# Kernel tuning notes

Hardware: AMD Instinct MI355X
Metric: run time of the kernel (lower is better)

Reference implementation:

```python
import jax, jax.numpy as jnp
import numpy as np

N_EMBED = 288
HEAD_SIZE = 32


def setup_inputs() -> dict:
    key = jax.random.key(0)
    kx, kk, kq, kv = jax.random.split(key, 4)
    B, T, C = 16, 2048, N_EMBED
    scale = 1.0 / np.sqrt(C)
    return {
        "x": jax.random.normal(kx, (B, T, C), dtype=jnp.float32),
        # Linear(n_embed, head_size, bias=False) weights, stored as [C, head_size]
        "Wk": jax.random.normal(kk, (C, HEAD_SIZE), dtype=jnp.float32) * scale,
        "Wq": jax.random.normal(kq, (C, HEAD_SIZE), dtype=jnp.float32) * scale,
        "Wv": jax.random.normal(kv, (C, HEAD_SIZE), dtype=jnp.float32) * scale,
    }


def reference(x, Wk, Wq, Wv):
    # x: [B, T, C]
    k = x @ Wk  # [B, T, hs]
    q = x @ Wq
    v = x @ Wv
    # NOTE: source computes k @ q^T (not q @ k^T) -- reproduce faithfully.
    weights = jnp.einsum("bth,bsh->bts", k, q) * (HEAD_SIZE ** -0.5)  # [B, T, T]
    T = x.shape[1]
    causal = jnp.tril(jnp.ones((T, T), dtype=bool))
    weights = jnp.where(causal, weights, -jnp.inf)
    weights = jax.nn.softmax(weights, axis=-1)
    return weights @ v  # [B, T, hs]
```

## Files before the change

kernel.cpp:

```cpp
#include <hip/hip_runtime.h>

typedef __bf16 bf16;
typedef __attribute__((ext_vector_type(8))) __bf16 bf16x8;
typedef __attribute__((ext_vector_type(4))) float f32x4;

#define BATCH 16
#define SEQ   2048
#define CEMB  288
#define HS    32
#define NROWS (BATCH * SEQ)

#define XSTR 296

__global__ __launch_bounds__(384, 3) void proj_kernel(
    const float* __restrict__ x, const float* __restrict__ Wk,
    const float* __restrict__ Wq, const float* __restrict__ Wv,
    bf16* __restrict__ Kx, bf16* __restrict__ Qm, bf16* __restrict__ VT)
{
    __shared__ __align__(16) bf16 Xl[32 * XSTR];

    const int tid  = threadIdx.x;
    const int wv   = tid >> 6;
    const int lane = tid & 63;
    const int quad = lane >> 4;
    const int ln   = lane & 15;
    const int dsel = wv >> 1;
    const int half = wv & 1;

    const float SCALE = 0.25519486439582695f;

    const float* Wsrc = (dsel == 0) ? Wk : ((dsel == 1) ? Wq : Wv);
    const float mul = (dsel == 0) ? SCALE : 1.0f;
    bf16x8 wfrag[9];
    for (int kc = 0; kc < 9; ++kc) {
        bf16x8 f;
#pragma unroll
        for (int j = 0; j < 8; ++j) {
            float w = Wsrc[(kc * 32 + quad * 8 + j) * HS + half * 16 + ln];
            f[j] = (bf16)(w * mul);
        }
        wfrag[kc] = f;
    }

    const int wgRowBase = blockIdx.x * 64;
    for (int it = 0; it < 2; ++it) {
        __syncthreads();
        const int rb = wgRowBase + it * 32;
#pragma unroll
        for (int i = 0; i < 6; ++i) {
            int f = tid + 384 * i;
            int row = f / 72;
            int c4  = f - row * 72;
            f32x4 v = ((const f32x4*)x)[(rb + row) * 72 + c4];
            bf16* d = &Xl[row * XSTR + c4 * 4];
            d[0] = (bf16)v[0]; d[1] = (bf16)v[1];
            d[2] = (bf16)v[2]; d[3] = (bf16)v[3];
        }
        __syncthreads();

#pragma unroll
        for (int m = 0; m < 2; ++m) {
            f32x4 acc = {0.f, 0.f, 0.f, 0.f};
#pragma unroll
            for (int kc = 0; kc < 9; ++kc) {
                bf16x8 a = *(const bf16x8*)&Xl[(m * 16 + ln) * XSTR + kc * 32 + quad * 8];
                acc = __builtin_amdgcn_mfma_f32_16x16x32_bf16(a, wfrag[kc], acc, 0, 0, 0);
            }
#pragma unroll
            for (int reg = 0; reg < 4; ++reg) {
                int gr = rb + m * 16 + quad * 4 + reg;
                bf16 val = (bf16)acc[reg];
                if (dsel == 0) {
                    Kx[gr * HS + half * 16 + ln] = val;
                } else if (dsel == 1) {
                    Qm[gr * HS + half * 16 + ln] = val;
                } else {
                    VT[(gr >> 11) * (HS * SEQ) + (half * 16 + ln) * SEQ + (gr & 2047)] = val;
                }
            }
        }
    }
}


__constant__ unsigned char MAP_TILE[40] = {
    4,5,6,7, 8,8,9,9, 10,10,11,11, 12,12,12, 13,13,13, 14,14,14, 15,15,15,
    3,7,11,15, 2,6,10,14, 1,5,9,13, 0,4,8,12 };
__constant__ unsigned char MAP_CHUNK[40] = {
    0,0,0,0, 0,1,0,1, 0,1,0,1, 0,1,2, 0,1,2, 0,1,2, 0,1,2,
    0,1,2,3, 0,1,2,3, 0,1,2,3, 0,1,2,3 };

__global__ __launch_bounds__(256, 4) void attn_kernel(
    const bf16* __restrict__ Kx, const bf16* __restrict__ Qm,
    const bf16* __restrict__ VT,
    float* __restrict__ Opart, float* __restrict__ Lpart)
{
    const int tid  = threadIdx.x;
    const int w    = tid >> 6;
    const int lane = tid & 63;
    const int quad = lane >> 4;
    const int ln   = lane & 15;

    const int bid   = blockIdx.x;
    const int u     = bid >> 4;
    const int b     = ((bid & 7) << 1) | ((bid >> 3) & 1);
    const int tile  = MAP_TILE[u];
    const int chunk = MAP_CHUNK[u];
    const int t0    = tile * 128;
    const int cs    = chunk * 512;
    const int ce    = min(cs + 512, t0 + 128);

    const bf16* Kb = Kx + b * SEQ * HS;
    const bf16* Qb = Qm + b * SEQ * HS;
    const bf16* Vb = VT + b * HS * SEQ;

    int tsub[2];
    bf16x8 kfrag[2];
#pragma unroll
    for (int m = 0; m < 2; ++m) {
        tsub[m] = t0 + w * 32 + m * 16;
        kfrag[m] = *(const bf16x8*)&Kb[(tsub[m] + ln) * HS + quad * 8];
    }
    bf16x8 ones;
#pragma unroll
    for (int j = 0; j < 8; ++j) ones[j] = (bf16)1.0f;

    const int qrow = 8 * (ln >> 2) + (ln & 3);
    const int t_row = ln;

    f32x4 Of[2][2] = {};
    f32x4 Lf[2]    = {};

    for (int s0 = cs; s0 < ce; s0 += 64) {
        if (s0 >= tsub[1] + 16) break;

        bf16x8 qfA[2], qfB[2];
#pragma unroll
        for (int c = 0; c < 2; ++c) {
            qfA[c] = *(const bf16x8*)&Qb[(s0 + 32 * c + qrow) * HS + quad * 8];
            qfB[c] = *(const bf16x8*)&Qb[(s0 + 32 * c + qrow + 4) * HS + quad * 8];
        }
        bf16x8 vf[2][2];
#pragma unroll
        for (int hb = 0; hb < 2; ++hb)
#pragma unroll
            for (int c = 0; c < 2; ++c)
                vf[hb][c] = *(const bf16x8*)&Vb[(hb * 16 + ln) * SEQ + s0 + c * 32 + quad * 8];

#pragma unroll
        for (int m = 0; m < 2; ++m) {
            const int t = tsub[m] + t_row;
#pragma unroll
            for (int c = 0; c < 2; ++c) {
                const int sb = s0 + 32 * c;
                if (sb >= tsub[m] + 16) continue;
                const bool diag = (sb + 31 > tsub[m]);

                f32x4 z = {0.f, 0.f, 0.f, 0.f};
                f32x4 SA = __builtin_amdgcn_mfma_f32_16x16x32_bf16(qfA[c], kfrag[m], z, 0, 0, 0);
                f32x4 SB = __builtin_amdgcn_mfma_f32_16x16x32_bf16(qfB[c], kfrag[m], z, 0, 0, 0);

                const int sAb = sb + 8 * quad;
                float pA[4], pB[4];
#pragma unroll
                for (int r = 0; r < 4; ++r) {
                    pA[r] = __builtin_amdgcn_exp2f(SA[r]);
                    pB[r] = __builtin_amdgcn_exp2f(SB[r]);
                    if (diag) {
                        pA[r] = (sAb + r     <= t) ? pA[r] : 0.0f;
                        pB[r] = (sAb + r + 4 <= t) ? pB[r] : 0.0f;
                    }
                }

                bf16x8 ap;
#pragma unroll
                for (int r = 0; r < 4; ++r) {
                    ap[r]     = (bf16)pA[r];
                    ap[r + 4] = (bf16)pB[r];
                }

                Of[m][0] = __builtin_amdgcn_mfma_f32_16x16x32_bf16(ap, vf[0][c], Of[m][0], 0, 0, 0);
                Of[m][1] = __builtin_amdgcn_mfma_f32_16x16x32_bf16(ap, vf[1][c], Of[m][1], 0, 0, 0);
                Lf[m]    = __builtin_amdgcn_mfma_f32_16x16x32_bf16(ap, ones,    Lf[m],    0, 0, 0);
            }
        }
    }

#pragma unroll
    for (int m = 0; m < 2; ++m) {
        if (cs >= tsub[m] + 16) continue;
#pragma unroll
        for (int reg = 0; reg < 4; ++reg) {
            int gr = b * SEQ + tsub[m] + quad * 4 + reg;
            float* od = Opart + ((size_t)chunk * NROWS + gr) * HS;
            od[ln]      = Of[m][0][reg];
            od[16 + ln] = Of[m][1][reg];
            if (ln == 0) Lpart[chunk * NROWS + gr] = Lf[m][reg];
        }
    }
}

__global__ __launch_bounds__(256) void combine_kernel(
    const float* __restrict__ Opart, const float* __restrict__ Lpart,
    float* __restrict__ out)
{
    int idx = blockIdx.x * 256 + threadIdx.x;
    int gr = idx >> 3, h4 = idx & 7;
    int t  = gr & 2047;
    int nc = (t >> 9) + 1;
    f32x4 acc = {0.f, 0.f, 0.f, 0.f};
    float l = 0.f;
    for (int c = 0; c < nc; ++c) {
        acc += ((const f32x4*)Opart)[((size_t)c * NROWS + gr) * 8 + h4];
        l   += Lpart[c * NROWS + gr];
    }
    f32x4 r = acc / l;
    ((f32x4*)out)[idx] = r;
}

extern "C" void kernel_launch(void* const* d_in, const int* in_sizes, int n_in,
                              void* d_out, int out_size, void* d_ws, size_t ws_size,
                              hipStream_t stream) {
    (void)in_sizes; (void)n_in; (void)out_size; (void)ws_size;
    const float* x  = (const float*)d_in[0];
    const float* Wk = (const float*)d_in[1];
    const float* Wq = (const float*)d_in[2];
    const float* Wv = (const float*)d_in[3];

    char* ws = (char*)d_ws;
    bf16*  Kx    = (bf16*)(ws);
    bf16*  Qm    = (bf16*)(ws + 2097152);
    bf16*  VT    = (bf16*)(ws + 4194304);
    float* Opart = (float*)(ws + 6291456);
    float* Lpart = (float*)(ws + 6291456 + 16777216);
    float* out   = (float*)d_out;

    hipLaunchKernelGGL(proj_kernel, dim3(512), dim3(384), 0, stream,
                       x, Wk, Wq, Wv, Kx, Qm, VT);
    hipLaunchKernelGGL(attn_kernel, dim3(640), dim3(256), 0, stream,
                       Kx, Qm, VT, Opart, Lpart);
    hipLaunchKernelGGL(combine_kernel, dim3(1024), dim3(256), 0, stream,
                       Opart, Lpart, out);
}
```

Measured before the change: 105.1 us.

## Use 1024-key split chunks and write unsplit rows directly to output

The key-axis split grows from 512 to 1024 columns, which cuts the number of (tile, chunk) work units from 40 to 24 per batch and the attention grid from 640 to 384 blocks. Tiles that fit in the first chunk now normalise and write straight to the output. The combine kernel only merges two partials for the second half of the sequence. This removes partial-buffer traffic and combine work, at the cost of fewer, longer blocks and possible load imbalance across CUs.

```diff
diff --git a/kernel.cpp b/kernel.cpp
--- a/kernel.cpp
+++ b/kernel.cpp
@@ -83,17 +83,18 @@
 }
 
 
-__constant__ unsigned char MAP_TILE[40] = {
-    4,5,6,7, 8,8,9,9, 10,10,11,11, 12,12,12, 13,13,13, 14,14,14, 15,15,15,
-    3,7,11,15, 2,6,10,14, 1,5,9,13, 0,4,8,12 };
-__constant__ unsigned char MAP_CHUNK[40] = {
-    0,0,0,0, 0,1,0,1, 0,1,0,1, 0,1,2, 0,1,2, 0,1,2, 0,1,2,
-    0,1,2,3, 0,1,2,3, 0,1,2,3, 0,1,2,3 };
+__constant__ unsigned char MAP_TILE[24] = {
+    7,8,9,10,11,12,13,14,15,15,
+    14,6, 13,5, 12,4, 11,3, 10,2, 9,1, 8,0 };
+__constant__ unsigned char MAP_CHUNK[24] = {
+    0,0,0,0,0,0,0,0,0,1,
+    1,0, 1,0, 1,0, 1,0, 1,0, 1,0, 1,0 };
 
 __global__ __launch_bounds__(256, 4) void attn_kernel(
     const bf16* __restrict__ Kx, const bf16* __restrict__ Qm,
     const bf16* __restrict__ VT,
-    float* __restrict__ Opart, float* __restrict__ Lpart)
+    float* __restrict__ Opart, float* __restrict__ Lpart,
+    float* __restrict__ out)
 {
     const int tid  = threadIdx.x;
     const int w    = tid >> 6;
@@ -107,8 +108,9 @@
     const int tile  = MAP_TILE[u];
     const int chunk = MAP_CHUNK[u];
     const int t0    = tile * 128;
-    const int cs    = chunk * 512;
-    const int ce    = min(cs + 512, t0 + 128);
+    const int cs    = chunk * 1024;
+    const int ce    = min(cs + 1024, t0 + 128);
+    const bool direct = (chunk == 0) && (t0 + 128 <= 1024);
 
     const bf16* Kb = Kx + b * SEQ * HS;
     const bf16* Qb = Qm + b * SEQ * HS;
@@ -189,13 +191,24 @@
 #pragma unroll
     for (int m = 0; m < 2; ++m) {
         if (cs >= tsub[m] + 16) continue;
-#pragma unroll
-        for (int reg = 0; reg < 4; ++reg) {
-            int gr = b * SEQ + tsub[m] + quad * 4 + reg;
-            float* od = Opart + ((size_t)chunk * NROWS + gr) * HS;
-            od[ln]      = Of[m][0][reg];
-            od[16 + ln] = Of[m][1][reg];
-            if (ln == 0) Lpart[chunk * NROWS + gr] = Lf[m][reg];
+        if (direct) {
+#pragma unroll
+            for (int reg = 0; reg < 4; ++reg) {
+                int gr = b * SEQ + tsub[m] + quad * 4 + reg;
+                float rl = 1.0f / Lf[m][reg];
+                float* od = out + (size_t)gr * HS;
+                od[ln]      = Of[m][0][reg] * rl;
+                od[16 + ln] = Of[m][1][reg] * rl;
+            }
+        } else {
+#pragma unroll
+            for (int reg = 0; reg < 4; ++reg) {
+                int gr = b * SEQ + tsub[m] + quad * 4 + reg;
+                float* od = Opart + ((size_t)chunk * NROWS + gr) * HS;
+                od[ln]      = Of[m][0][reg];
+                od[16 + ln] = Of[m][1][reg];
+                if (ln == 0) Lpart[chunk * NROWS + gr] = Lf[m][reg];
+            }
         }
     }
 }
@@ -205,17 +218,13 @@
     float* __restrict__ out)
 {
     int idx = blockIdx.x * 256 + threadIdx.x;
-    int gr = idx >> 3, h4 = idx & 7;
-    int t  = gr & 2047;
-    int nc = (t >> 9) + 1;
-    f32x4 acc = {0.f, 0.f, 0.f, 0.f};
-    float l = 0.f;
-    for (int c = 0; c < nc; ++c) {
-        acc += ((const f32x4*)Opart)[((size_t)c * NROWS + gr) * 8 + h4];
-        l   += Lpart[c * NROWS + gr];
-    }
-    f32x4 r = acc / l;
-    ((f32x4*)out)[idx] = r;
+    int row = idx >> 3, h4 = idx & 7;
+    int bb  = row >> 10, r = row & 1023;
+    int gr  = bb * SEQ + 1024 + r;
+    f32x4 acc = ((const f32x4*)Opart)[(size_t)gr * 8 + h4]
+              + ((const f32x4*)Opart)[((size_t)NROWS + gr) * 8 + h4];
+    float l = Lpart[gr] + Lpart[NROWS + gr];
+    ((f32x4*)out)[(size_t)gr * 8 + h4] = acc / l;
 }
 
 extern "C" void kernel_launch(void* const* d_in, const int* in_sizes, int n_in,
@@ -232,13 +241,13 @@
     bf16*  Qm    = (bf16*)(ws + 2097152);
     bf16*  VT    = (bf16*)(ws + 4194304);
     float* Opart = (float*)(ws + 6291456);
-    float* Lpart = (float*)(ws + 6291456 + 16777216);
+    float* Lpart = (float*)(ws + 6291456 + 8388608);
     float* out   = (float*)d_out;
 
     hipLaunchKernelGGL(proj_kernel, dim3(512), dim3(384), 0, stream,
                        x, Wk, Wq, Wv, Kx, Qm, VT);
-    hipLaunchKernelGGL(attn_kernel, dim3(640), dim3(256), 0, stream,
-                       Kx, Qm, VT, Opart, Lpart);
-    hipLaunchKernelGGL(combine_kernel, dim3(1024), dim3(256), 0, stream,
+    hipLaunchKernelGGL(attn_kernel, dim3(384), dim3(256), 0, stream,
+                       Kx, Qm, VT, Opart, Lpart, out);
+    hipLaunchKernelGGL(combine_kernel, dim3(512), dim3(256), 0, stream,
                        Opart, Lpart, out);
 }
```

After: 108.3 us. 3.1% more time.
